# Performance work log

Hardware: AMD Instinct MI355X
Metric: run time of the kernel (lower is better)

Reference implementation:

```python
import jax, jax.numpy as jnp
import numpy as np
import math

N, D = 4096, 1024


def setup_inputs() -> dict:
    key = jax.random.key(0)
    ks = jax.random.split(key, 8)
    vecs = jax.random.normal(ks[0], (N, D), dtype=jnp.float32)
    mass = jax.random.uniform(ks[1], (N,), dtype=jnp.float32)            # semantic mass in [0,1)
    hops = jax.random.uniform(ks[2], (N,), dtype=jnp.float32) * 5.0      # hop distances in [0,5)
    alive = jax.random.randint(ks[3], (N,), 0, 10) > 0
    is_photon = jax.random.randint(ks[4], (N,), 0, 10) == 0
    W_res_w = jax.random.normal(ks[5], (D, D), dtype=jnp.float32) / np.sqrt(D)
    W_res_b = jnp.zeros((D,), dtype=jnp.float32)
    w_conf_i = jax.random.normal(ks[6], (D,), dtype=jnp.float32) / np.sqrt(2 * D)
    w_conf_j = jax.random.normal(ks[7], (D,), dtype=jnp.float32) / np.sqrt(2 * D)
    b_conf = jnp.zeros((), dtype=jnp.float32)
    log_c = jnp.asarray(math.log(50.0), dtype=jnp.float32)  # 'relationship' domain
    log_G = jnp.zeros((), dtype=jnp.float32)
    return dict(vecs=vecs, mass=mass, hops=hops, alive=alive, is_photon=is_photon,
                W_res_w=W_res_w, W_res_b=W_res_b, w_conf_i=w_conf_i, w_conf_j=w_conf_j,
                b_conf=b_conf, log_c=log_c, log_G=log_G)


def reference(vecs, mass, hops, alive, is_photon, W_res_w, W_res_b,
              w_conf_i, w_conf_j, b_conf, log_c, log_G):
    n = vecs.shape[0]
    c = jnp.maximum(jnp.exp(log_c), 1e-6)
    G = jnp.exp(log_G)

    # Per-row quantities (phi() reads hops/photon from entity i).
    d_light = hops / c                                                   # [N]
    lam = jnp.where(is_photon, 1.0, jnp.exp(-d_light))                   # redshift, [N]
    r2 = jnp.maximum(d_light, 0.1) ** 2                                  # r_safe^2, [N]
    causal_decay = jnp.where(d_light <= 1.0, 1.0, jnp.exp(-d_light + 1.0))  # [N]

    # Causal mask: j must be strictly in the past (j < i).
    idx = jnp.arange(n)
    past = (idx[None, :] < idx[:, None]).astype(vecs.dtype)              # [N,N]
    C = past * causal_decay[:, None]

    # Gravity: G * m_i * m_j / r_i^2
    grav = G * (mass / r2)[:, None] * mass[None, :]                      # [N,N]

    # Resonance: cosine similarity of W_res projections (torch eps=1e-8 norm clamp).
    v = vecs @ W_res_w.T + W_res_b                                       # [N,D]
    vn = v / jnp.maximum(jnp.linalg.norm(v, axis=-1, keepdims=True), 1e-8)
    R = vn @ vn.T                                                        # [N,N]
    zero_norm = jnp.linalg.norm(vecs, axis=-1) < 1e-8                    # [N]
    R = jnp.where(zero_norm[:, None] | zero_norm[None, :], 0.0, R)

    # Conflict gate: sigmoid(W_conflict @ concat(v_i, v_j) + b) = sigmoid(s_i + s_j + b).
    s_i = vecs @ w_conf_i                                                # [N]
    s_j = vecs @ w_conf_j                                                # [N]
    conflict = jax.nn.sigmoid(s_i[:, None] + s_j[None, :] + b_conf)      # [N,N]

    phi_attract = lam[:, None] * grav * C * (0.5 + 0.5 * R)
    phi_repulse = -lam[:, None] * conflict * mass[:, None] * mass[None, :]
    phi = jnp.where(conflict > 0.8, phi_repulse, phi_attract)

    # Black holes and the diagonal produce zero field.
    gate = alive[:, None] & alive[None, :]
    phi = jnp.where(gate & (idx[:, None] != idx[None, :]), phi, 0.0)
    return phi
```

## Files before the change

kernel.cpp:

```cpp
#include <hip/hip_runtime.h>
#include <hip/hip_bf16.h>
#include <math.h>

#define NROW 4096
#define DIM  1024

typedef short v8s __attribute__((ext_vector_type(8)));
typedef float v4f __attribute__((ext_vector_type(4)));

__device__ __forceinline__ ushort f2bf(float f) {
    __hip_bfloat16 h = __float2bfloat16(f);
    union { __hip_bfloat16 h; ushort u; } x; x.h = h; return x.u;
}

__global__ __launch_bounds__(256) void k_rowstats(
    const float* __restrict__ vecs, const float* __restrict__ mass,
    const float* __restrict__ hops, const int* __restrict__ alive,
    const int* __restrict__ is_photon, const float* __restrict__ wci,
    const float* __restrict__ wcj, const float* __restrict__ logc,
    const float* __restrict__ logG,
    double* __restrict__ s_i, double* __restrict__ s_j,
    float* __restrict__ rowAtt, float* __restrict__ rowRep,
    float* __restrict__ massF, int* __restrict__ flags)
{
    const int row = blockIdx.x, t = threadIdx.x;
    const float* vr = vecs + (size_t)row * DIM;
    const int base = t * 4;
    float4 pv = *(const float4*)&vr[base];
    float4 pi = *(const float4*)&wci[base];
    float4 pj = *(const float4*)&wcj[base];
    double di = (double)pv.x * pi.x + (double)pv.y * pi.y + (double)pv.z * pi.z + (double)pv.w * pi.w;
    double dj = (double)pv.x * pj.x + (double)pv.y * pj.y + (double)pv.z * pj.z + (double)pv.w * pj.w;
    double ss = (double)pv.x * pv.x + (double)pv.y * pv.y + (double)pv.z * pv.z + (double)pv.w * pv.w;
    #pragma unroll
    for (int off = 32; off > 0; off >>= 1) {
        di += __shfl_down(di, off);
        dj += __shfl_down(dj, off);
        ss += __shfl_down(ss, off);
    }
    __shared__ double rd[3][4];
    const int wid = t >> 6;
    if ((t & 63) == 0) { rd[0][wid] = di; rd[1][wid] = dj; rd[2][wid] = ss; }
    __syncthreads();
    if (t == 0) {
        di = rd[0][0] + rd[0][1] + rd[0][2] + rd[0][3];
        dj = rd[1][0] + rd[1][1] + rd[1][2] + rd[1][3];
        ss = rd[2][0] + rd[2][1] + rd[2][2] + rd[2][3];
        double c  = fmax(exp((double)logc[0]), 1e-6);
        double G  = exp((double)logG[0]);
        double dl = (double)hops[row] / c;
        double lam = (is_photon[row] != 0) ? 1.0 : exp(-dl);
        double rs  = fmax(dl, 0.1);
        double cd  = (dl <= 1.0) ? 1.0 : exp(-dl + 1.0);
        double m   = (double)mass[row];
        s_i[row] = di;
        s_j[row] = dj;
        rowAtt[row] = (float)(lam * G * m / (rs * rs) * cd);
        rowRep[row] = (float)(-lam * m);
        massF[row]  = (float)m;
        flags[row]  = ((alive[row] != 0) ? 1 : 0) | ((sqrt(ss) < 1e-8) ? 2 : 0);
    }
}

__global__ __launch_bounds__(256) void k_proj(
    const float* __restrict__ A, const float* __restrict__ B,
    const float* __restrict__ bias, ushort* __restrict__ vout)
{
    __shared__ ushort As[128 * 32], Bs[128 * 32];
    const int t = threadIdx.x;
    const int m0 = blockIdx.y * 128, n0 = blockIdx.x * 128;
    const int wid = t >> 6, lane = t & 63;
    const int wm = wid >> 1, wn = wid & 1;
    const int quad = lane >> 4, l16 = lane & 15;
    v4f acc[4][4];
    #pragma unroll
    for (int i = 0; i < 4; i++)
        #pragma unroll
        for (int j = 0; j < 4; j++) acc[i][j] = (v4f){0.f, 0.f, 0.f, 0.f};

    for (int k0 = 0; k0 < DIM; k0 += 32) {
        #pragma unroll
        for (int p = 0; p < 4; ++p) {
            int c = p * 256 + t;
            int r = c >> 3, co = (c & 7) * 4;
            float4 fa = *(const float4*)&A[(size_t)(m0 + r) * DIM + k0 + co];
            float4 fb = *(const float4*)&B[(size_t)(n0 + r) * DIM + k0 + co];
            ushort4 ua, ub;
            ua.x = f2bf(fa.x); ua.y = f2bf(fa.y); ua.z = f2bf(fa.z); ua.w = f2bf(fa.w);
            ub.x = f2bf(fb.x); ub.y = f2bf(fb.y); ub.z = f2bf(fb.z); ub.w = f2bf(fb.w);
            *(ushort4*)&As[r * 32 + co] = ua;
            *(ushort4*)&Bs[r * 32 + co] = ub;
        }
        __syncthreads();
        v8s af[4], bfr[4];
        #pragma unroll
        for (int mi = 0; mi < 4; mi++) af[mi]  = *(const v8s*)&As[(wm * 64 + mi * 16 + l16) * 32 + quad * 8];
        #pragma unroll
        for (int ni = 0; ni < 4; ni++) bfr[ni] = *(const v8s*)&Bs[(wn * 64 + ni * 16 + l16) * 32 + quad * 8];
        #pragma unroll
        for (int mi = 0; mi < 4; mi++)
            #pragma unroll
            for (int ni = 0; ni < 4; ni++)
                acc[mi][ni] = __builtin_amdgcn_mfma_f32_16x16x32_bf16(af[mi], bfr[ni], acc[mi][ni], 0, 0, 0);
        __syncthreads();
    }
    float bcol[4];
    #pragma unroll
    for (int ni = 0; ni < 4; ni++) bcol[ni] = bias[n0 + wn * 64 + ni * 16 + l16];
    #pragma unroll
    for (int mi = 0; mi < 4; mi++)
        #pragma unroll
        for (int r = 0; r < 4; r++) {
            int row = m0 + wm * 64 + mi * 16 + quad * 4 + r;
            #pragma unroll
            for (int ni = 0; ni < 4; ni++) {
                int col = n0 + wn * 64 + ni * 16 + l16;
                vout[(size_t)row * DIM + col] = f2bf(acc[mi][ni][r] + bcol[ni]);
            }
        }
}

__global__ __launch_bounds__(256) void k_norm(ushort* __restrict__ v)
{
    const int row = blockIdx.x, t = threadIdx.x;
    ushort* vr = v + (size_t)row * DIM;
    ushort4 pv = *(const ushort4*)&vr[t * 4];
    union { unsigned i; float f; } c0, c1, c2, c3;
    c0.i = ((unsigned)pv.x) << 16; c1.i = ((unsigned)pv.y) << 16;
    c2.i = ((unsigned)pv.z) << 16; c3.i = ((unsigned)pv.w) << 16;
    float x0 = c0.f, x1 = c1.f, x2 = c2.f, x3 = c3.f;
    float ss = x0 * x0 + x1 * x1 + x2 * x2 + x3 * x3;
    #pragma unroll
    for (int off = 32; off > 0; off >>= 1) ss += __shfl_down(ss, off);
    __shared__ float r4[4];
    __shared__ float sinv;
    if ((t & 63) == 0) r4[t >> 6] = ss;
    __syncthreads();
    if (t == 0) sinv = 1.0f / fmaxf(sqrtf(r4[0] + r4[1] + r4[2] + r4[3]), 1e-8f);
    __syncthreads();
    float inv = sinv;
    ushort4 o;
    o.x = f2bf(x0 * inv); o.y = f2bf(x1 * inv); o.z = f2bf(x2 * inv); o.w = f2bf(x3 * inv);
    *(ushort4*)&vr[t * 4] = o;
}

__global__ __launch_bounds__(256) void k_phi(
    const ushort* __restrict__ vn,
    const double* __restrict__ s_i, const double* __restrict__ s_j,
    const float* __restrict__ rowAtt, const float* __restrict__ rowRep,
    const float* __restrict__ massF, const int* __restrict__ flags,
    const float* __restrict__ bconf_p, float* __restrict__ out)
{
    __shared__ ushort As[128 * 32], Bs[128 * 32];
    const int t = threadIdx.x;
    const int bi = blockIdx.y, bj = blockIdx.x;
    const int m0 = bi * 128, n0 = bj * 128;
    const int wid = t >> 6, lane = t & 63;
    const int wm = wid >> 1, wn = wid & 1;
    const int quad = lane >> 4, l16 = lane & 15;
    v4f acc[4][4];
    #pragma unroll
    for (int i = 0; i < 4; i++)
        #pragma unroll
        for (int j = 0; j < 4; j++) acc[i][j] = (v4f){0.f, 0.f, 0.f, 0.f};

    if (bi >= bj) {
        for (int k0 = 0; k0 < DIM; k0 += 32) {
            #pragma unroll
            for (int p = 0; p < 2; ++p) {
                int c = p * 256 + t;
                int r = c >> 2, co = (c & 3) * 8;
                *(uint4*)&As[r * 32 + co] = *(const uint4*)&vn[(size_t)(m0 + r) * DIM + k0 + co];
                *(uint4*)&Bs[r * 32 + co] = *(const uint4*)&vn[(size_t)(n0 + r) * DIM + k0 + co];
            }
            __syncthreads();
            v8s af[4], bfr[4];
            #pragma unroll
            for (int mi = 0; mi < 4; mi++) af[mi]  = *(const v8s*)&As[(wm * 64 + mi * 16 + l16) * 32 + quad * 8];
            #pragma unroll
            for (int ni = 0; ni < 4; ni++) bfr[ni] = *(const v8s*)&Bs[(wn * 64 + ni * 16 + l16) * 32 + quad * 8];
            #pragma unroll
            for (int mi = 0; mi < 4; mi++)
                #pragma unroll
                for (int ni = 0; ni < 4; ni++)
                    acc[mi][ni] = __builtin_amdgcn_mfma_f32_16x16x32_bf16(af[mi], bfr[ni], acc[mi][ni], 0, 0, 0);
            __syncthreads();
        }
    }

    const double bc  = (double)bconf_p[0];
    const double LN4 = 1.3862943611198906;
    float  cm[4]; double csj[4]; int cf[4]; int ccol[4];
    #pragma unroll
    for (int ni = 0; ni < 4; ni++) {
        int col = n0 + wn * 64 + ni * 16 + l16;
        ccol[ni] = col; cm[ni] = massF[col]; csj[ni] = s_j[col]; cf[ni] = flags[col];
    }
    #pragma unroll
    for (int mi = 0; mi < 4; mi++)
        #pragma unroll
        for (int r = 0; r < 4; r++) {
            int row = m0 + wm * 64 + mi * 16 + quad * 4 + r;
            float  rA = rowAtt[row], rR = rowRep[row];
            int    fi = flags[row];
            double si = s_i[row];
            size_t ob = (size_t)row * NROW;
            #pragma unroll
            for (int ni = 0; ni < 4; ni++) {
                int col = ccol[ni];
                double x = si + csj[ni] + bc;
                float conflict = 1.0f / (1.0f + expf(-(float)x));
                bool  chigh = x > LN4;
                bool  gate  = ((fi & cf[ni]) & 1) && (row != col);
                float Rv  = ((fi | cf[ni]) & 2) ? 0.0f : acc[mi][ni][r];
                float att = (col < row) ? rA * cm[ni] * (0.5f + 0.5f * Rv) : 0.0f;
                float ph  = gate ? (chigh ? rR * conflict * cm[ni] : att) : 0.0f;
                out[ob + col] = ph;
            }
        }
}

extern "C" void kernel_launch(void* const* d_in, const int* in_sizes, int n_in,
                              void* d_out, int out_size, void* d_ws, size_t ws_size,
                              hipStream_t stream)
{
    const float* vecs      = (const float*)d_in[0];
    const float* mass      = (const float*)d_in[1];
    const float* hops      = (const float*)d_in[2];
    const int*   alive     = (const int*)d_in[3];
    const int*   is_photon = (const int*)d_in[4];
    const float* W         = (const float*)d_in[5];
    const float* Wb        = (const float*)d_in[6];
    const float* wci       = (const float*)d_in[7];
    const float* wcj       = (const float*)d_in[8];
    const float* bconf     = (const float*)d_in[9];
    const float* logc      = (const float*)d_in[10];
    const float* logG      = (const float*)d_in[11];

    char* ws = (char*)d_ws;
    double* s_i    = (double*)(ws);
    double* s_j    = (double*)(ws + 32768);
    float*  rowAtt = (float*)(ws + 65536);
    float*  rowRep = (float*)(ws + 81920);
    float*  massF  = (float*)(ws + 98304);
    int*    flagsA = (int*)(ws + 114688);
    ushort* vn     = (ushort*)(ws + 131072);

    k_rowstats<<<dim3(NROW), dim3(256), 0, stream>>>(
        vecs, mass, hops, alive, is_photon, wci, wcj, logc, logG,
        s_i, s_j, rowAtt, rowRep, massF, flagsA);
    k_proj<<<dim3(DIM / 128, NROW / 128), dim3(256), 0, stream>>>(vecs, W, Wb, vn);
    k_norm<<<dim3(NROW), dim3(256), 0, stream>>>(vn);
    k_phi<<<dim3(NROW / 128, NROW / 128), dim3(256), 0, stream>>>(
        vn, s_i, s_j, rowAtt, rowRep, massF, flagsA, bconf, (float*)d_out);
}
```

Baseline: 208.6 us.

## Interleave heavy and light phi tiles on a 1D grid, load tiles via global_load_lds

Replaces the 2D 32x32 tile grid with a 1D grid of 1024 blocks. The 528 lower-triangle tiles, which run the GMMA, are interleaved with the 496 upper-triangle tiles, which only write output, so that work spreads evenly across CUs instead of bunching by launch order. The A/B tile loads now use global_load_lds, which copies straight from global memory into LDS and skips the register round trip. The cost is a loop-based index decode per block and a dependence on the LDS layout produced by the direct-to-LDS lane mapping.

```diff
diff --git a/kernel.cpp b/kernel.cpp
--- a/kernel.cpp
+++ b/kernel.cpp
@@ -153,7 +153,22 @@
 {
     __shared__ ushort As[128 * 32], Bs[128 * 32];
     const int t = threadIdx.x;
-    const int bi = blockIdx.y, bj = blockIdx.x;
+    const int id = blockIdx.x;
+
+    const int h  = (id * 528) >> 10;
+    const int h2 = ((id + 1) * 528) >> 10;
+    const bool heavy = (h2 > h);
+    int bi, bj;
+    if (heavy) {
+        int r = 0;
+        while (h >= ((r + 1) * (r + 2)) >> 1) ++r;
+        bi = r; bj = h - ((r * (r + 1)) >> 1);
+    } else {
+        int l = id - h;
+        int r = 0;
+        while (l >= 31 - r) { l -= 31 - r; ++r; }
+        bi = r; bj = r + 1 + l;
+    }
     const int m0 = bi * 128, n0 = bj * 128;
     const int wid = t >> 6, lane = t & 63;
     const int wm = wid >> 1, wn = wid & 1;
@@ -164,14 +179,20 @@
         #pragma unroll
         for (int j = 0; j < 4; j++) acc[i][j] = (v4f){0.f, 0.f, 0.f, 0.f};
 
-    if (bi >= bj) {
+    if (heavy) {
         for (int k0 = 0; k0 < DIM; k0 += 32) {
             #pragma unroll
             for (int p = 0; p < 2; ++p) {
-                int c = p * 256 + t;
+                int c = (wid * 2 + p) * 64 + lane;
                 int r = c >> 2, co = (c & 3) * 8;
-                *(uint4*)&As[r * 32 + co] = *(const uint4*)&vn[(size_t)(m0 + r) * DIM + k0 + co];
-                *(uint4*)&Bs[r * 32 + co] = *(const uint4*)&vn[(size_t)(n0 + r) * DIM + k0 + co];
+                const ushort* ga = &vn[(size_t)(m0 + r) * DIM + k0 + co];
+                const ushort* gb = &vn[(size_t)(n0 + r) * DIM + k0 + co];
+                __builtin_amdgcn_global_load_lds(
+                    (const __attribute__((address_space(1))) void*)ga,
+                    (__attribute__((address_space(3))) void*)&As[(wid * 2 + p) * 512], 16, 0, 0);
+                __builtin_amdgcn_global_load_lds(
+                    (const __attribute__((address_space(1))) void*)gb,
+                    (__attribute__((address_space(3))) void*)&Bs[(wid * 2 + p) * 512], 16, 0, 0);
             }
             __syncthreads();
             v8s af[4], bfr[4];
@@ -251,6 +272,6 @@
         s_i, s_j, rowAtt, rowRep, massF, flagsA);
     k_proj<<<dim3(DIM / 128, NROW / 128), dim3(256), 0, stream>>>(vecs, W, Wb, vn);
     k_norm<<<dim3(NROW), dim3(256), 0, stream>>>(vn);
-    k_phi<<<dim3(NROW / 128, NROW / 128), dim3(256), 0, stream>>>(
+    k_phi<<<dim3(1024), dim3(256), 0, stream>>>(
         vn, s_i, s_j, rowAtt, rowRep, massF, flagsA, bconf, (float*)d_out);
 }
```

New measurement: 204.5 us. Within noise of the previous version (-1.9%).
